# Optimization experiments

Hardware: AMD Instinct MI355X
Metric: run time of the kernel (lower is better)

Reference implementation:

```python
import jax, jax.numpy as jnp
import numpy as np

D_EMBED = 512
NUM_HEADS = 8
HEAD_DIM = D_EMBED // NUM_HEADS
D_FF = 2048
B, L = 2, 4096
LN_EPS = 1e-5


def _layernorm(x, g, b):
    mu = jnp.mean(x, axis=-1, keepdims=True)
    var = jnp.mean(jnp.square(x - mu), axis=-1, keepdims=True)
    return (x - mu) * jax.lax.rsqrt(var + LN_EPS) * g + b


def setup_inputs() -> dict:
    key = jax.random.key(0)
    ks = jax.random.split(key, 16)
    s = 0.02
    inp = {
        "x": jax.random.normal(ks[0], (B, L, D_EMBED), dtype=jnp.float32),
        "mask": jnp.ones((B, 1, 1, L), dtype=jnp.int32),
        # attention projections (stored [in, out] for x @ W)
        "Wq": jax.random.normal(ks[1], (D_EMBED, D_EMBED), dtype=jnp.float32) * s,
        "bq": jnp.zeros((D_EMBED,), dtype=jnp.float32),
        "Wk": jax.random.normal(ks[2], (D_EMBED, D_EMBED), dtype=jnp.float32) * s,
        "bk": jnp.zeros((D_EMBED,), dtype=jnp.float32),
        "Wv": jax.random.normal(ks[3], (D_EMBED, D_EMBED), dtype=jnp.float32) * s,
        "bv": jnp.zeros((D_EMBED,), dtype=jnp.float32),
        "Wo": jax.random.normal(ks[4], (D_EMBED, D_EMBED), dtype=jnp.float32) * s,
        "bo": jnp.zeros((D_EMBED,), dtype=jnp.float32),
        # layernorms
        "ln1_g": jnp.ones((D_EMBED,), dtype=jnp.float32),
        "ln1_b": jnp.zeros((D_EMBED,), dtype=jnp.float32),
        "ln2_g": jnp.ones((D_EMBED,), dtype=jnp.float32),
        "ln2_b": jnp.zeros((D_EMBED,), dtype=jnp.float32),
        # FFN
        "W1": jax.random.normal(ks[5], (D_EMBED, D_FF), dtype=jnp.float32) * s,
        "b1": jnp.zeros((D_FF,), dtype=jnp.float32),
        "W2": jax.random.normal(ks[6], (D_FF, D_EMBED), dtype=jnp.float32) * s,
        "b2": jnp.zeros((D_EMBED,), dtype=jnp.float32),
    }
    return inp


def reference(x, mask, Wq, bq, Wk, bk, Wv, bv, Wo, bo, ln1_g, ln1_b,
              W1, b1, W2, b2, ln2_g, ln2_b):
    Bx, Lx, _ = x.shape
    # projections -> [B, H, L, Dh]
    def split_heads(t):
        return t.reshape(Bx, Lx, NUM_HEADS, HEAD_DIM).transpose(0, 2, 1, 3)
    q = split_heads(x @ Wq + bq)
    k = split_heads(x @ Wk + bk)
    v = split_heads(x @ Wv + bv)
    scores = jnp.einsum("bhqd,bhkd->bhqk", q, k) / jnp.sqrt(
        jnp.asarray(HEAD_DIM, dtype=x.dtype))
    scores = jnp.where(mask == 0, jnp.asarray(-1e9, dtype=x.dtype), scores)
    attn = jax.nn.softmax(scores, axis=-1)
    ctx = jnp.einsum("bhqk,bhkd->bhqd", attn, v)
    ctx = ctx.transpose(0, 2, 1, 3).reshape(Bx, Lx, D_EMBED)
    attn_out = ctx @ Wo + bo

    h = _layernorm(x + attn_out, ln1_g, ln1_b)
    ff = (jax.nn.gelu(h @ W1 + b1, approximate=False)) @ W2 + b2
    return _layernorm(h + ff, ln2_g, ln2_b)
```

## Files before the change

### kernel.cpp

```cpp
#include <hip/hip_runtime.h>
#include <hip/hip_bf16.h>
#include <math.h>

#define D_EMBED 512
#define NUM_HEADS 8
#define HEAD_DIM 64
#define D_FF 2048
#define BATCH 2
#define SEQ 4096
#define M_ROWS (BATCH*SEQ)
#define QSCALE 0.18033688011112042f

typedef __attribute__((ext_vector_type(8))) short short8;
typedef __attribute__((ext_vector_type(4))) short short4_t;
typedef __attribute__((ext_vector_type(4))) float f32x4;

#if __has_builtin(__builtin_amdgcn_mfma_f32_16x16x16bf16_1k)
#define MFMA_K16(a,b,c) __builtin_amdgcn_mfma_f32_16x16x16bf16_1k(a,b,c,0,0,0)
#elif __has_builtin(__builtin_amdgcn_mfma_f32_16x16x16_bf16)
#define MFMA_K16(a,b,c) __builtin_amdgcn_mfma_f32_16x16x16_bf16(a,b,c,0,0,0)
#else
#define MFMA_K16(a,b,c) (c)
#endif

#if __has_builtin(__builtin_amdgcn_exp2f)
#define EXP2(x) __builtin_amdgcn_exp2f(x)
#else
#define EXP2(x) exp2f(x)
#endif

__device__ inline unsigned short f2b(float f) {
    union { float f; unsigned u; } v; v.f = f;
    unsigned r = v.u + 0x7fffu + ((v.u >> 16) & 1u);
    return (unsigned short)(r >> 16);
}

__device__ inline float b2f(short s) {
    union { unsigned u; float f; } v;
    v.u = ((unsigned)(unsigned short)s) << 16;
    return v.f;
}

__device__ inline short4_t pk4(float p0, float p1, float p2, float p3) {
    union { __hip_bfloat162 h2[2]; short4_t s4; } u;
    u.h2[0] = __float22bfloat162_rn(make_float2(p0, p1));
    u.h2[1] = __float22bfloat162_rn(make_float2(p2, p3));
    return u.s4;
}

__device__ inline void gl2lds16(const void* g, void* l) {
    __builtin_amdgcn_global_load_lds(
        (const __attribute__((address_space(1))) unsigned int*)g,
        (__attribute__((address_space(3))) unsigned int*)l, 16, 0, 0);
}

template<int EPI>
__global__ __launch_bounds__(256) void gemm_bt(
    const unsigned short* __restrict__ A, const unsigned short* __restrict__ BT,
    const float* __restrict__ bias, void* __restrict__ Cout,
    int M, int N, int K, int scale_cols)
{
    __shared__ __align__(16) unsigned short As[128*32];
    __shared__ __align__(16) unsigned short Bs[128*32];
    const int tid  = threadIdx.x;
    const int wave = tid >> 6, lane = tid & 63;
    const int wy = wave >> 1, wx = wave & 1;
    const int quad = lane >> 4, m16 = lane & 15;
    const int row0 = blockIdx.y * 128, n0 = blockIdx.x * 128;
    const int rdoff = (quad ^ ((m16 >> 1) & 3)) * 8;

    f32x4 acc[4][4];
#pragma unroll
    for (int i = 0; i < 4; i++)
#pragma unroll
        for (int j = 0; j < 4; j++) acc[i][j] = (f32x4){0.f,0.f,0.f,0.f};

    const int kIters = K >> 5;
    for (int kt = 0; kt < kIters; ++kt) {
        const int k0 = kt << 5;
#pragma unroll
        for (int it = 0; it < 2; ++it) {
            int g  = it*256 + tid;
            int r  = g >> 2;
            int c8 = (((g & 3) ^ ((g >> 3) & 3)) << 3);
            gl2lds16(A  + (size_t)(row0 + r)*K + k0 + c8, &As[(size_t)(it*256 + wave*64)*8]);
            gl2lds16(BT + (size_t)(n0  + r)*K + k0 + c8, &Bs[(size_t)(it*256 + wave*64)*8]);
        }
        __syncthreads();
        short8 a[4], b[4];
#pragma unroll
        for (int i = 0; i < 4; i++) a[i] = *(const short8*)&As[(wy*64 + i*16 + m16)*32 + rdoff];
#pragma unroll
        for (int j = 0; j < 4; j++) b[j] = *(const short8*)&Bs[(wx*64 + j*16 + m16)*32 + rdoff];
#pragma unroll
        for (int i = 0; i < 4; i++)
#pragma unroll
            for (int j = 0; j < 4; j++)
                acc[i][j] = __builtin_amdgcn_mfma_f32_16x16x32_bf16(a[i], b[j], acc[i][j], 0, 0, 0);
        __syncthreads();
    }

#pragma unroll
    for (int j = 0; j < 4; j++) {
        int col = n0 + wx*64 + j*16 + m16;
        float bj = bias[col];
        float sc = (col < scale_cols) ? QSCALE : 1.0f;
#pragma unroll
        for (int i = 0; i < 4; i++) {
            int rbase = row0 + wy*64 + i*16 + quad*4;
#pragma unroll
            for (int r = 0; r < 4; r++) {
                float v = (acc[i][j][r] + bj) * sc;
                size_t idx = (size_t)(rbase + r)*N + col;
                if (EPI == 0) {
                    ((unsigned short*)Cout)[idx] = f2b(v);
                } else if (EPI == 1) {
                    ((float*)Cout)[idx] = v;
                } else {
                    float gv = 0.5f * v * (1.0f + erff(v * 0.70710678118654752f));
                    ((unsigned short*)Cout)[idx] = f2b(gv);
                }
            }
        }
    }
}

template<int EPI>
__global__ __launch_bounds__(256) void gemm_bt64(
    const unsigned short* __restrict__ A, const unsigned short* __restrict__ BT,
    const float* __restrict__ bias, void* __restrict__ Cout,
    int M, int N, int K, int scale_cols)
{
    __shared__ __align__(16) unsigned short As[64*32];
    __shared__ __align__(16) unsigned short Bs[128*32];
    const int tid  = threadIdx.x;
    const int wave = tid >> 6, lane = tid & 63;
    const int wy = wave >> 1, wx = wave & 1;
    const int quad = lane >> 4, m16 = lane & 15;
    const int row0 = blockIdx.y * 64, n0 = blockIdx.x * 128;
    const int rdoff = (quad ^ ((m16 >> 1) & 3)) * 8;

    f32x4 acc[2][4];
#pragma unroll
    for (int i = 0; i < 2; i++)
#pragma unroll
        for (int j = 0; j < 4; j++) acc[i][j] = (f32x4){0.f,0.f,0.f,0.f};

    const int kIters = K >> 5;
    for (int kt = 0; kt < kIters; ++kt) {
        const int k0 = kt << 5;
        {
            int r = tid >> 2;
            int c8 = (((tid & 3) ^ ((tid >> 3) & 3)) << 3);
            gl2lds16(A + (size_t)(row0 + r)*K + k0 + c8, &As[(size_t)(wave*64)*8]);
        }
#pragma unroll
        for (int it = 0; it < 2; ++it) {
            int g  = it*256 + tid;
            int r  = g >> 2;
            int c8 = (((g & 3) ^ ((g >> 3) & 3)) << 3);
            gl2lds16(BT + (size_t)(n0 + r)*K + k0 + c8, &Bs[(size_t)(it*256 + wave*64)*8]);
        }
        __syncthreads();
        short8 a[2], b[4];
#pragma unroll
        for (int i = 0; i < 2; i++) a[i] = *(const short8*)&As[(wy*32 + i*16 + m16)*32 + rdoff];
#pragma unroll
        for (int j = 0; j < 4; j++) b[j] = *(const short8*)&Bs[(wx*64 + j*16 + m16)*32 + rdoff];
#pragma unroll
        for (int i = 0; i < 2; i++)
#pragma unroll
            for (int j = 0; j < 4; j++)
                acc[i][j] = __builtin_amdgcn_mfma_f32_16x16x32_bf16(a[i], b[j], acc[i][j], 0, 0, 0);
        __syncthreads();
    }

#pragma unroll
    for (int j = 0; j < 4; j++) {
        int col = n0 + wx*64 + j*16 + m16;
        float bj = bias[col];
        float sc = (col < scale_cols) ? QSCALE : 1.0f;
#pragma unroll
        for (int i = 0; i < 2; i++) {
            int rbase = row0 + wy*32 + i*16 + quad*4;
#pragma unroll
            for (int r = 0; r < 4; r++) {
                float v = (acc[i][j][r] + bj) * sc;
                size_t idx = (size_t)(rbase + r)*N + col;
                if (EPI == 0) {
                    ((unsigned short*)Cout)[idx] = f2b(v);
                } else if (EPI == 1) {
                    ((float*)Cout)[idx] = v;
                } else {
                    float gv = 0.5f * v * (1.0f + erff(v * 0.70710678118654752f));
                    ((unsigned short*)Cout)[idx] = f2b(gv);
                }
            }
        }
    }
}

__global__ __launch_bounds__(256) void repack_qk(
    const unsigned short* __restrict__ QKV,
    unsigned short* __restrict__ Qp, unsigned short* __restrict__ Kp)
{
    const int bh = blockIdx.y, b = bh >> 3, h = bh & 7;
    const int l0 = blockIdx.x * 64;
    const int t = threadIdx.x;
    const int row = t >> 2, c = (t & 3) * 16;
    const unsigned short* src = QKV + (size_t)(b*SEQ + l0 + row)*1536 + h*64 + c;
    const size_t dst = ((size_t)bh*SEQ + l0 + row)*64 + c;
    *(short8*)&Qp[dst]   = *(const short8*)(src);
    *(short8*)&Qp[dst+8] = *(const short8*)(src + 8);
    *(short8*)&Kp[dst]   = *(const short8*)(src + 512);
    *(short8*)&Kp[dst+8] = *(const short8*)(src + 520);
}

__global__ __launch_bounds__(256) void transpose_v2(
    const unsigned short* __restrict__ QKV, unsigned short* __restrict__ Vp)
{
    __shared__ unsigned short Ls[128][66];
    const int kt = blockIdx.x, bh = blockIdx.y, b = bh >> 3, h = bh & 7;
    const int t = threadIdx.x;
    {
        int key = t >> 1, dhalf = (t & 1) * 32;
        const unsigned short* src =
            QKV + (size_t)(b*SEQ + kt*128 + key)*1536 + 1024 + h*64 + dhalf;
#pragma unroll
        for (int c = 0; c < 4; ++c)
            *(short8*)&Ls[key][dhalf + c*8] = *(const short8*)(src + c*8);
    }
    __syncthreads();
    {
        int quad = t >> 6, d = t & 63;
        unsigned short tmp[32];
#pragma unroll
        for (int nj = 0; nj < 8; ++nj)
#pragma unroll
            for (int r = 0; r < 4; ++r)
                tmp[nj*4 + r] = Ls[nj*16 + quad*4 + r][d];
        unsigned short* dst = Vp + ((((size_t)bh*32 + kt)*4 + quad)*64 + d)*32;
#pragma unroll
        for (int c = 0; c < 4; ++c)
            *(short8*)&dst[c*8] = *(const short8*)&tmp[c*8];
    }
}

__global__ void mask_flags_k(const int* __restrict__ mask, int* __restrict__ flags)
{
    int t = threadIdx.x;
    const int* m = mask + t*128;
    int all = 1;
    for (int i = 0; i < 128; i += 4) {
        int4 v = *(const int4*)(m + i);
        all &= (v.x && v.y && v.z && v.w) ? 1 : 0;
    }
    flags[t] = all;
}

__global__ __launch_bounds__(256) void kmax_k(
    const unsigned short* __restrict__ Kp, float* __restrict__ kmax)
{
    const int bh = blockIdx.x, t = threadIdx.x;
    const int wave = t >> 6, lane = t & 63;
    float mx = 0.f;
    for (int row = t; row < SEQ; row += 256) {
        const unsigned short* kp = Kp + ((size_t)bh*SEQ + row)*64;
        float s = 0.f;
#pragma unroll
        for (int c = 0; c < 8; ++c) {
            short8 v = *(const short8*)(kp + c*8);
#pragma unroll
            for (int j = 0; j < 8; ++j) { float f = b2f(v[j]); s += f*f; }
        }
        mx = fmaxf(mx, s);
    }
#pragma unroll
    for (int off = 32; off >= 1; off >>= 1)
        mx = fmaxf(mx, __shfl_xor(mx, off, 64));
    __shared__ float w[4];
    if (lane == 0) w[wave] = mx;
    __syncthreads();
    if (t == 0)
        kmax[bh] = sqrtf(fmaxf(fmaxf(w[0], w[1]), fmaxf(w[2], w[3])));
}

__global__ __launch_bounds__(256) void flash_attn(
    const unsigned short* __restrict__ Qp, const unsigned short* __restrict__ Kp,
    const unsigned short* __restrict__ Vp, const int* __restrict__ mask,
    const int* __restrict__ flags, const float* __restrict__ kmax,
    unsigned short* __restrict__ O)
{
    __shared__ __align__(16) unsigned short Ks[2][128*32];
    __shared__ __align__(16) unsigned short Vs[4][64*32];
    const int tid = threadIdx.x, wave = tid >> 6, lane = tid & 63;
    const int quad = lane >> 4, m16 = lane & 15;
    const int bh = blockIdx.y, b = bh >> 3, h = bh & 7;
    const int qbase = blockIdx.x * 64 + wave * 16;
    const int fsw = (m16 >> 1) & 3;
    const int koff = (quad ^ fsw) * 8;

    const unsigned short* Qb = Qp + (size_t)bh*SEQ*64;
    const unsigned short* Kb = Kp + (size_t)bh*SEQ*64;
    const unsigned short* Vb = Vp + (size_t)bh*32*4*64*32;
    const int* mbase = mask + b*SEQ;
    const int* fbase = flags + b*(SEQ/128);

    short8 qf[2];
    {
        const unsigned short* qp = Qb + (size_t)(qbase + m16)*64 + quad*8;
        qf[0] = *(const short8*)qp;
        qf[1] = *(const short8*)(qp + 32);
    }
    float qn2 = 0.f;
#pragma unroll
    for (int j = 0; j < 8; ++j) {
        float f0 = b2f(qf[0][j]), f1 = b2f(qf[1][j]);
        qn2 += f0*f0 + f1*f1;
    }
    qn2 += __shfl_xor(qn2, 16, 64);
    qn2 += __shfl_xor(qn2, 32, 64);
    const float M = sqrtf(qn2) * kmax[bh];

    f32x4 accO[4];
#pragma unroll
    for (int dj = 0; dj < 4; dj++) accO[dj] = (f32x4){0.f,0.f,0.f,0.f};
    float rs = 0.f;

    for (int kt = 0; kt < SEQ/128; ++kt) {
        const int key0 = kt * 128;
        const int allones = fbase[kt];
        __syncthreads();
#pragma unroll
        for (int it = 0; it < 2; ++it) {
            int g = it*256 + tid;
            int r = g >> 2;
            int c8 = (((g & 3) ^ ((g >> 3) & 3)) << 3);
            gl2lds16(Kb + (size_t)(key0 + r)*64 + c8,      &Ks[0][(it*256 + wave*64)*8]);
            gl2lds16(Kb + (size_t)(key0 + r)*64 + 32 + c8, &Ks[1][(it*256 + wave*64)*8]);
        }
        {
            int d = wave*16 + (lane >> 2), ch = lane & 3;
            int c8 = (ch ^ ((d >> 1) & 3)) * 8;
#pragma unroll
            for (int qr = 0; qr < 4; ++qr)
                gl2lds16(Vb + (((size_t)kt*4 + qr)*64 + d)*32 + c8,
                         &Vs[qr][wave*64*8]);
        }
        __syncthreads();

        short4_t pb[8];
#pragma unroll
        for (int nj = 0; nj < 8; ++nj) {
            short8 k0 = *(const short8*)&Ks[0][(nj*16 + m16)*32 + koff];
            short8 k1 = *(const short8*)&Ks[1][(nj*16 + m16)*32 + koff];
            f32x4 c = (f32x4){0.f,0.f,0.f,0.f};
            c = __builtin_amdgcn_mfma_f32_16x16x32_bf16(k0, qf[0], c, 0, 0, 0);
            c = __builtin_amdgcn_mfma_f32_16x16x32_bf16(k1, qf[1], c, 0, 0, 0);
            if (!allones) {
                int4 mv = *(const int4*)(mbase + key0 + nj*16 + quad*4);
                c[0] = mv.x ? c[0] : -1e9f;
                c[1] = mv.y ? c[1] : -1e9f;
                c[2] = mv.z ? c[2] : -1e9f;
                c[3] = mv.w ? c[3] : -1e9f;
            }
            float p0 = EXP2(c[0] - M);
            float p1 = EXP2(c[1] - M);
            float p2 = EXP2(c[2] - M);
            float p3 = EXP2(c[3] - M);
            rs += (p0 + p1) + (p2 + p3);
            pb[nj] = pk4(p0, p1, p2, p3);
        }

#pragma unroll
        for (int l = 0; l < 4; ++l) {
#pragma unroll
            for (int dj = 0; dj < 4; ++dj) {
                short8 vv = *(const short8*)
                    &Vs[quad][(dj*16 + m16)*32 + ((l ^ fsw) * 8)];
                short4_t vlo = __builtin_shufflevector(vv, vv, 0, 1, 2, 3);
                short4_t vhi = __builtin_shufflevector(vv, vv, 4, 5, 6, 7);
                accO[dj] = MFMA_K16(vlo, pb[2*l],     accO[dj]);
                accO[dj] = MFMA_K16(vhi, pb[2*l + 1], accO[dj]);
            }
        }
    }

    rs += __shfl_xor(rs, 16, 64);
    rs += __shfl_xor(rs, 32, 64);
    float rl = 1.0f / rs;
#pragma unroll
    for (int dj = 0; dj < 4; ++dj) {
        short4_t o = pk4(accO[dj][0]*rl, accO[dj][1]*rl,
                         accO[dj][2]*rl, accO[dj][3]*rl);
        *(short4_t*)&O[(size_t)(b*SEQ + qbase + m16)*D_EMBED
                       + h*HEAD_DIM + dj*16 + quad*4] = o;
    }
}

__global__ __launch_bounds__(256) void ln_res(
    const float* __restrict__ A, const unsigned short* __restrict__ Bv,
    const float* __restrict__ g, const float* __restrict__ be,
    float* __restrict__ Yf, unsigned short* __restrict__ Yb)
{
    const int wave = threadIdx.x >> 6, lane = threadIdx.x & 63;
    const int row = blockIdx.x * 4 + wave;
    const float* ap = A + (size_t)row*512 + lane*8;
    short8 bv = *(const short8*)(Bv + (size_t)row*512 + lane*8);
    float v[8]; float s = 0.f;
#pragma unroll
    for (int j = 0; j < 8; j++) { v[j] = ap[j] + b2f(bv[j]); s += v[j]; }
#pragma unroll
    for (int off = 32; off >= 1; off >>= 1) s += __shfl_xor(s, off, 64);
    float mu = s * (1.f/512.f);
    float q = 0.f;
#pragma unroll
    for (int j = 0; j < 8; j++) { v[j] -= mu; q += v[j]*v[j]; }
#pragma unroll
    for (int off = 32; off >= 1; off >>= 1) q += __shfl_xor(q, off, 64);
    float rstd = rsqrtf(q * (1.f/512.f) + 1e-5f);
#pragma unroll
    for (int j = 0; j < 8; j++) {
        float y = v[j]*rstd*g[lane*8+j] + be[lane*8+j];
        if (Yf) Yf[(size_t)row*512 + lane*8 + j] = y;
        if (Yb) Yb[(size_t)row*512 + lane*8 + j] = f2b(y);
    }
}

__global__ __launch_bounds__(256) void cvt_f32_bf16(
    const float* __restrict__ X, unsigned short* __restrict__ Y, int n)
{
    int idx = (blockIdx.x * 256 + threadIdx.x) * 4;
    if (idx < n) {
        float4 v = *(const float4*)(X + idx);
        Y[idx+0] = f2b(v.x); Y[idx+1] = f2b(v.y);
        Y[idx+2] = f2b(v.z); Y[idx+3] = f2b(v.w);
    }
}

__global__ void transpose_w(const float* __restrict__ W, unsigned short* __restrict__ WT,
                            int K, int N)
{
    __shared__ float t[32][33];
    int n0 = blockIdx.x*32, k0 = blockIdx.y*32;
    int x = threadIdx.x, y = threadIdx.y;
#pragma unroll
    for (int yy = y; yy < 32; yy += 8) t[yy][x] = W[(size_t)(k0+yy)*N + n0 + x];
    __syncthreads();
#pragma unroll
    for (int yy = y; yy < 32; yy += 8) WT[(size_t)(n0+yy)*K + k0 + x] = f2b(t[x][yy]);
}

__global__ void concat3(const float* __restrict__ a, const float* __restrict__ b,
                        const float* __restrict__ c, float* __restrict__ o)
{
    int i = blockIdx.x*256 + threadIdx.x;
    o[i] = (i < 512) ? a[i] : ((i < 1024) ? b[i-512] : c[i-1024]);
}

extern "C" void kernel_launch(void* const* d_in, const int* in_sizes, int n_in,
                              void* d_out, int out_size, void* d_ws, size_t ws_size,
                              hipStream_t stream)
{
    const float* x    = (const float*)d_in[0];
    const int*   mask = (const int*)  d_in[1];
    const float* Wq = (const float*)d_in[2];  const float* bq = (const float*)d_in[3];
    const float* Wk = (const float*)d_in[4];  const float* bk = (const float*)d_in[5];
    const float* Wv = (const float*)d_in[6];  const float* bv = (const float*)d_in[7];
    const float* Wo = (const float*)d_in[8];  const float* bo = (const float*)d_in[9];
    const float* ln1g = (const float*)d_in[10]; const float* ln1b = (const float*)d_in[11];
    const float* ln2g = (const float*)d_in[12]; const float* ln2b = (const float*)d_in[13];
    const float* W1 = (const float*)d_in[14]; const float* b1 = (const float*)d_in[15];
    const float* W2 = (const float*)d_in[16]; const float* b2 = (const float*)d_in[17];
    float* out = (float*)d_out;

    char* ws = (char*)d_ws;
    const size_t MB = 1024*1024;
    unsigned short* xb    = (unsigned short*)(ws + 0);
    unsigned short* WqkvT = (unsigned short*)(ws + 8*MB);
    unsigned short* W1T   = (unsigned short*)(ws + 10*MB);
    unsigned short* W2T   = (unsigned short*)(ws + 12*MB);
    unsigned short* WoT   = (unsigned short*)(ws + 14*MB);
    float*          bqkv  = (float*)(ws + 14*MB + 512*1024);
    int*            mflag = (int*)(ws + 14*MB + 768*1024);
    float*          kmaxb = (float*)(ws + 14*MB + 772*1024);
    unsigned short* QKVb  = (unsigned short*)(ws + 15*MB);
    unsigned short* Qp    = (unsigned short*)(ws + 39*MB);
    unsigned short* Kp    = (unsigned short*)(ws + 47*MB);
    unsigned short* Vp    = (unsigned short*)(ws + 55*MB);
    unsigned short* ctx   = (unsigned short*)(ws + 63*MB);
    unsigned short* atfb  = (unsigned short*)(ws + 15*MB);
    unsigned short* ffb   = (unsigned short*)(ws + 23*MB);
    float*          hf    = (float*)(ws + 31*MB);
    unsigned short* hb    = (unsigned short*)(ws + 0);
    unsigned short* Gb    = (unsigned short*)(ws + 47*MB);

    dim3 tb(32, 8);
    cvt_f32_bf16<<<4096, 256, 0, stream>>>(x, xb, M_ROWS*D_EMBED);
    transpose_w<<<dim3(16,16), tb, 0, stream>>>(Wq, WqkvT,            512, 512);
    transpose_w<<<dim3(16,16), tb, 0, stream>>>(Wk, WqkvT + 512*512,  512, 512);
    transpose_w<<<dim3(16,16), tb, 0, stream>>>(Wv, WqkvT + 1024*512, 512, 512);
    transpose_w<<<dim3(16,16), tb, 0, stream>>>(Wo, WoT, 512, 512);
    transpose_w<<<dim3(64,16), tb, 0, stream>>>(W1, W1T, 512, 2048);
    transpose_w<<<dim3(16,64), tb, 0, stream>>>(W2, W2T, 2048, 512);
    concat3<<<6, 256, 0, stream>>>(bq, bk, bv, bqkv);
    mask_flags_k<<<1, 64, 0, stream>>>(mask, mflag);

    gemm_bt<0><<<dim3(12,64), 256, 0, stream>>>(xb, WqkvT, bqkv, QKVb, M_ROWS, 1536, 512, 512);

    repack_qk<<<dim3(SEQ/64, 16), 256, 0, stream>>>(QKVb, Qp, Kp);
    transpose_v2<<<dim3(32, 16), 256, 0, stream>>>(QKVb, Vp);
    kmax_k<<<16, 256, 0, stream>>>(Kp, kmaxb);
    flash_attn<<<dim3(SEQ/64, 16), 256, 0, stream>>>(Qp, Kp, Vp, mask, mflag, kmaxb, ctx);

    gemm_bt64<0><<<dim3(4,128), 256, 0, stream>>>(ctx, WoT, bo, atfb, M_ROWS, 512, 512, 0);
    ln_res<<<M_ROWS/4, 256, 0, stream>>>(x, atfb, ln1g, ln1b, hf, hb);

    gemm_bt<2><<<dim3(16,64), 256, 0, stream>>>(hb, W1T, b1, Gb, M_ROWS, D_FF, 512, 0);
    gemm_bt64<0><<<dim3(4,128), 256, 0, stream>>>(Gb, W2T, b2, ffb, M_ROWS, 512, D_FF, 0);
    ln_res<<<M_ROWS/4, 256, 0, stream>>>(hf, ffb, ln2g, ln2b, out, (unsigned short*)nullptr);
}
```

Measured before the change: 431.4 us.

## Fuse QKV head repack and V transpose into QKV GEMM epilogue

```diff
diff --git a/kernel.cpp b/kernel.cpp
--- a/kernel.cpp
+++ b/kernel.cpp
@@ -58,7 +58,7 @@
 __global__ __launch_bounds__(256) void gemm_bt(
     const unsigned short* __restrict__ A, const unsigned short* __restrict__ BT,
     const float* __restrict__ bias, void* __restrict__ Cout,
-    int M, int N, int K, int scale_cols)
+    int M, int N, int K)
 {
     __shared__ __align__(16) unsigned short As[128*32];
     __shared__ __align__(16) unsigned short Bs[128*32];
@@ -104,18 +104,15 @@
     for (int j = 0; j < 4; j++) {
         int col = n0 + wx*64 + j*16 + m16;
         float bj = bias[col];
-        float sc = (col < scale_cols) ? QSCALE : 1.0f;
 #pragma unroll
         for (int i = 0; i < 4; i++) {
             int rbase = row0 + wy*64 + i*16 + quad*4;
 #pragma unroll
             for (int r = 0; r < 4; r++) {
-                float v = (acc[i][j][r] + bj) * sc;
+                float v = acc[i][j][r] + bj;
                 size_t idx = (size_t)(rbase + r)*N + col;
                 if (EPI == 0) {
                     ((unsigned short*)Cout)[idx] = f2b(v);
-                } else if (EPI == 1) {
-                    ((float*)Cout)[idx] = v;
                 } else {
                     float gv = 0.5f * v * (1.0f + erff(v * 0.70710678118654752f));
                     ((unsigned short*)Cout)[idx] = f2b(gv);
@@ -125,11 +122,86 @@
     }
 }
 
-template<int EPI>
+__global__ __launch_bounds__(256) void gemm_qkv(
+    const unsigned short* __restrict__ A, const unsigned short* __restrict__ BT,
+    const float* __restrict__ bias,
+    unsigned short* __restrict__ Qp, unsigned short* __restrict__ Kp,
+    unsigned short* __restrict__ Vp)
+{
+    const int K = 512, N = 1536;
+    __shared__ __align__(16) unsigned short As[128*32];
+    __shared__ __align__(16) unsigned short Bs[128*32];
+    const int tid  = threadIdx.x;
+    const int wave = tid >> 6, lane = tid & 63;
+    const int wy = wave >> 1, wx = wave & 1;
+    const int quad = lane >> 4, m16 = lane & 15;
+    const int row0 = blockIdx.y * 128, n0 = blockIdx.x * 128;
+    const int rdoff = (quad ^ ((m16 >> 1) & 3)) * 8;
+    const int region = n0 >> 9;
+
+    f32x4 acc[4][4];
+#pragma unroll
+    for (int i = 0; i < 4; i++)
+#pragma unroll
+        for (int j = 0; j < 4; j++) acc[i][j] = (f32x4){0.f,0.f,0.f,0.f};
+
+    for (int kt = 0; kt < 16; ++kt) {
+        const int k0 = kt << 5;
+#pragma unroll
+        for (int it = 0; it < 2; ++it) {
+            int g  = it*256 + tid;
+            int r  = g >> 2;
+            int c8 = (((g & 3) ^ ((g >> 3) & 3)) << 3);
+            gl2lds16(A  + (size_t)(row0 + r)*K + k0 + c8, &As[(size_t)(it*256 + wave*64)*8]);
+            gl2lds16(BT + (size_t)(n0  + r)*K + k0 + c8, &Bs[(size_t)(it*256 + wave*64)*8]);
+        }
+        __syncthreads();
+        short8 a[4], b[4];
+#pragma unroll
+        for (int i = 0; i < 4; i++) a[i] = *(const short8*)&As[(wy*64 + i*16 + m16)*32 + rdoff];
+#pragma unroll
+        for (int j = 0; j < 4; j++) b[j] = *(const short8*)&Bs[(wx*64 + j*16 + m16)*32 + rdoff];
+#pragma unroll
+        for (int i = 0; i < 4; i++)
+#pragma unroll
+            for (int j = 0; j < 4; j++)
+                acc[i][j] = __builtin_amdgcn_mfma_f32_16x16x32_bf16(a[i], b[j], acc[i][j], 0, 0, 0);
+        __syncthreads();
+    }
+
+    const float sc = (region == 0) ? QSCALE : 1.0f;
+#pragma unroll
+    for (int j = 0; j < 4; j++) {
+        int col = n0 + wx*64 + j*16 + m16;
+        float bj = bias[col];
+        int cc = col & 511, h = cc >> 6, d = cc & 63;
+#pragma unroll
+        for (int i = 0; i < 4; i++) {
+            int rbase = row0 + wy*64 + i*16 + quad*4;
+#pragma unroll
+            for (int r = 0; r < 4; r++) {
+                float v = (acc[i][j][r] + bj) * sc;
+                int row = rbase + r;
+                int b = row >> 12, l = row & 4095;
+                size_t bh = (size_t)(b*8 + h);
+                if (region == 0) {
+                    Qp[(bh*SEQ + l)*64 + d] = f2b(v);
+                } else if (region == 1) {
+                    Kp[(bh*SEQ + l)*64 + d] = f2b(v);
+                } else {
+                    int kt = l >> 7, kk = l & 127;
+                    int qr = (kk >> 2) & 3, fi = (kk >> 4)*4 + (kk & 3);
+                    Vp[((((bh*32 + kt)*4 + qr)*64 + d)*32) + fi] = f2b(v);
+                }
+            }
+        }
+    }
+}
+
 __global__ __launch_bounds__(256) void gemm_bt64(
     const unsigned short* __restrict__ A, const unsigned short* __restrict__ BT,
-    const float* __restrict__ bias, void* __restrict__ Cout,
-    int M, int N, int K, int scale_cols)
+    const float* __restrict__ bias, unsigned short* __restrict__ Cout,
+    int M, int N, int K)
 {
     __shared__ __align__(16) unsigned short As[64*32];
     __shared__ __align__(16) unsigned short Bs[128*32];
@@ -179,70 +251,15 @@
     for (int j = 0; j < 4; j++) {
         int col = n0 + wx*64 + j*16 + m16;
         float bj = bias[col];
-        float sc = (col < scale_cols) ? QSCALE : 1.0f;
 #pragma unroll
         for (int i = 0; i < 2; i++) {
             int rbase = row0 + wy*32 + i*16 + quad*4;
 #pragma unroll
             for (int r = 0; r < 4; r++) {
-                float v = (acc[i][j][r] + bj) * sc;
-                size_t idx = (size_t)(rbase + r)*N + col;
-                if (EPI == 0) {
-                    ((unsigned short*)Cout)[idx] = f2b(v);
-                } else if (EPI == 1) {
-                    ((float*)Cout)[idx] = v;
-                } else {
-                    float gv = 0.5f * v * (1.0f + erff(v * 0.70710678118654752f));
-                    ((unsigned short*)Cout)[idx] = f2b(gv);
-                }
+                float v = acc[i][j][r] + bj;
+                Cout[(size_t)(rbase + r)*N + col] = f2b(v);
             }
         }
-    }
-}
-
-__global__ __launch_bounds__(256) void repack_qk(
-    const unsigned short* __restrict__ QKV,
-    unsigned short* __restrict__ Qp, unsigned short* __restrict__ Kp)
-{
-    const int bh = blockIdx.y, b = bh >> 3, h = bh & 7;
-    const int l0 = blockIdx.x * 64;
-    const int t = threadIdx.x;
-    const int row = t >> 2, c = (t & 3) * 16;
-    const unsigned short* src = QKV + (size_t)(b*SEQ + l0 + row)*1536 + h*64 + c;
-    const size_t dst = ((size_t)bh*SEQ + l0 + row)*64 + c;
-    *(short8*)&Qp[dst]   = *(const short8*)(src);
-    *(short8*)&Qp[dst+8] = *(const short8*)(src + 8);
-    *(short8*)&Kp[dst]   = *(const short8*)(src + 512);
-    *(short8*)&Kp[dst+8] = *(const short8*)(src + 520);
-}
-
-__global__ __launch_bounds__(256) void transpose_v2(
-    const unsigned short* __restrict__ QKV, unsigned short* __restrict__ Vp)
-{
-    __shared__ unsigned short Ls[128][66];
-    const int kt = blockIdx.x, bh = blockIdx.y, b = bh >> 3, h = bh & 7;
-    const int t = threadIdx.x;
-    {
-        int key = t >> 1, dhalf = (t & 1) * 32;
-        const unsigned short* src =
-            QKV + (size_t)(b*SEQ + kt*128 + key)*1536 + 1024 + h*64 + dhalf;
-#pragma unroll
-        for (int c = 0; c < 4; ++c)
-            *(short8*)&Ls[key][dhalf + c*8] = *(const short8*)(src + c*8);
-    }
-    __syncthreads();
-    {
-        int quad = t >> 6, d = t & 63;
-        unsigned short tmp[32];
-#pragma unroll
-        for (int nj = 0; nj < 8; ++nj)
-#pragma unroll
-            for (int r = 0; r < 4; ++r)
-                tmp[nj*4 + r] = Ls[nj*16 + quad*4 + r][d];
-        unsigned short* dst = Vp + ((((size_t)bh*32 + kt)*4 + quad)*64 + d)*32;
-#pragma unroll
-        for (int c = 0; c < 4; ++c)
-            *(short8*)&dst[c*8] = *(const short8*)&tmp[c*8];
     }
 }
 
@@ -259,36 +276,28 @@
 }
 
 __global__ __launch_bounds__(256) void kmax_k(
-    const unsigned short* __restrict__ Kp, float* __restrict__ kmax)
+    const unsigned short* __restrict__ Kp, unsigned* __restrict__ kmax2)
 {
     const int bh = blockIdx.x, t = threadIdx.x;
-    const int wave = t >> 6, lane = t & 63;
-    float mx = 0.f;
-    for (int row = t; row < SEQ; row += 256) {
-        const unsigned short* kp = Kp + ((size_t)bh*SEQ + row)*64;
-        float s = 0.f;
-#pragma unroll
-        for (int c = 0; c < 8; ++c) {
-            short8 v = *(const short8*)(kp + c*8);
-#pragma unroll
-            for (int j = 0; j < 8; ++j) { float f = b2f(v[j]); s += f*f; }
-        }
-        mx = fmaxf(mx, s);
+    const int row = blockIdx.y*256 + t;
+    const unsigned short* kp = Kp + ((size_t)bh*SEQ + row)*64;
+    float s = 0.f;
+#pragma unroll
+    for (int c = 0; c < 8; ++c) {
+        short8 v = *(const short8*)(kp + c*8);
+#pragma unroll
+        for (int j = 0; j < 8; ++j) { float f = b2f(v[j]); s += f*f; }
     }
 #pragma unroll
     for (int off = 32; off >= 1; off >>= 1)
-        mx = fmaxf(mx, __shfl_xor(mx, off, 64));
-    __shared__ float w[4];
-    if (lane == 0) w[wave] = mx;
-    __syncthreads();
-    if (t == 0)
-        kmax[bh] = sqrtf(fmaxf(fmaxf(w[0], w[1]), fmaxf(w[2], w[3])));
+        s = fmaxf(s, __shfl_xor(s, off, 64));
+    if ((t & 63) == 0) atomicMax(&kmax2[bh], __float_as_uint(s));
 }
 
 __global__ __launch_bounds__(256) void flash_attn(
     const unsigned short* __restrict__ Qp, const unsigned short* __restrict__ Kp,
     const unsigned short* __restrict__ Vp, const int* __restrict__ mask,
-    const int* __restrict__ flags, const float* __restrict__ kmax,
+    const int* __restrict__ flags, const unsigned* __restrict__ kmax2,
     unsigned short* __restrict__ O)
 {
     __shared__ __align__(16) unsigned short Ks[2][128*32];
@@ -320,7 +329,7 @@
     }
     qn2 += __shfl_xor(qn2, 16, 64);
     qn2 += __shfl_xor(qn2, 32, 64);
-    const float M = sqrtf(qn2) * kmax[bh];
+    const float M = sqrtf(qn2 * __uint_as_float(kmax2[bh]));
 
     f32x4 accO[4];
 #pragma unroll
@@ -376,10 +385,9 @@
         for (int l = 0; l < 4; ++l) {
 #pragma unroll
             for (int dj = 0; dj < 4; ++dj) {
-                short8 vv = *(const short8*)
-                    &Vs[quad][(dj*16 + m16)*32 + ((l ^ fsw) * 8)];
-                short4_t vlo = __builtin_shufflevector(vv, vv, 0, 1, 2, 3);
-                short4_t vhi = __builtin_shufflevector(vv, vv, 4, 5, 6, 7);
+                const unsigned short* vrow = &Vs[quad][(dj*16 + m16)*32 + ((l ^ fsw) * 8)];
+                short4_t vlo = *(const short4_t*)vrow;
+                short4_t vhi = *(const short4_t*)(vrow + 4);
                 accO[dj] = MFMA_K16(vlo, pb[2*l],     accO[dj]);
                 accO[dj] = MFMA_K16(vhi, pb[2*l + 1], accO[dj]);
             }
@@ -483,17 +491,16 @@
     unsigned short* WoT   = (unsigned short*)(ws + 14*MB);
     float*          bqkv  = (float*)(ws + 14*MB + 512*1024);
     int*            mflag = (int*)(ws + 14*MB + 768*1024);
-    float*          kmaxb = (float*)(ws + 14*MB + 772*1024);
-    unsigned short* QKVb  = (unsigned short*)(ws + 15*MB);
-    unsigned short* Qp    = (unsigned short*)(ws + 39*MB);
-    unsigned short* Kp    = (unsigned short*)(ws + 47*MB);
-    unsigned short* Vp    = (unsigned short*)(ws + 55*MB);
-    unsigned short* ctx   = (unsigned short*)(ws + 63*MB);
-    unsigned short* atfb  = (unsigned short*)(ws + 15*MB);
-    unsigned short* ffb   = (unsigned short*)(ws + 23*MB);
-    float*          hf    = (float*)(ws + 31*MB);
+    unsigned*       kmaxb = (unsigned*)(ws + 14*MB + 772*1024);
+    unsigned short* Qp    = (unsigned short*)(ws + 15*MB);
+    unsigned short* Kp    = (unsigned short*)(ws + 23*MB);
+    unsigned short* Vp    = (unsigned short*)(ws + 31*MB);
+    unsigned short* ctx   = (unsigned short*)(ws + 39*MB);
+    unsigned short* atfb  = (unsigned short*)(ws + 47*MB);
+    float*          hf    = (float*)(ws + 55*MB);
     unsigned short* hb    = (unsigned short*)(ws + 0);
-    unsigned short* Gb    = (unsigned short*)(ws + 47*MB);
+    unsigned short* Gb    = (unsigned short*)(ws + 15*MB);
+    unsigned short* ffb   = (unsigned short*)(ws + 47*MB);
 
     dim3 tb(32, 8);
     cvt_f32_bf16<<<4096, 256, 0, stream>>>(x, xb, M_ROWS*D_EMBED);
@@ -505,18 +512,17 @@
     transpose_w<<<dim3(16,64), tb, 0, stream>>>(W2, W2T, 2048, 512);
     concat3<<<6, 256, 0, stream>>>(bq, bk, bv, bqkv);
     mask_flags_k<<<1, 64, 0, stream>>>(mask, mflag);
-
-    gemm_bt<0><<<dim3(12,64), 256, 0, stream>>>(xb, WqkvT, bqkv, QKVb, M_ROWS, 1536, 512, 512);
-
-    repack_qk<<<dim3(SEQ/64, 16), 256, 0, stream>>>(QKVb, Qp, Kp);
-    transpose_v2<<<dim3(32, 16), 256, 0, stream>>>(QKVb, Vp);
-    kmax_k<<<16, 256, 0, stream>>>(Kp, kmaxb);
+    hipMemsetAsync(kmaxb, 0, 16*sizeof(unsigned), stream);
+
+    gemm_qkv<<<dim3(12,64), 256, 0, stream>>>(xb, WqkvT, bqkv, Qp, Kp, Vp);
+
+    kmax_k<<<dim3(16,16), 256, 0, stream>>>(Kp, kmaxb);
     flash_attn<<<dim3(SEQ/64, 16), 256, 0, stream>>>(Qp, Kp, Vp, mask, mflag, kmaxb, ctx);
 
-    gemm_bt64<0><<<dim3(4,128), 256, 0, stream>>>(ctx, WoT, bo, atfb, M_ROWS, 512, 512, 0);
+    gemm_bt64<<<dim3(4,128), 256, 0, stream>>>(ctx, WoT, bo, atfb, M_ROWS, 512, 512);
     ln_res<<<M_ROWS/4, 256, 0, stream>>>(x, atfb, ln1g, ln1b, hf, hb);
 
-    gemm_bt<2><<<dim3(16,64), 256, 0, stream>>>(hb, W1T, b1, Gb, M_ROWS, D_FF, 512, 0);
-    gemm_bt64<0><<<dim3(4,128), 256, 0, stream>>>(Gb, W2T, b2, ffb, M_ROWS, 512, D_FF, 0);
+    gemm_bt<2><<<dim3(16,64), 256, 0, stream>>>(hb, W1T, b1, Gb, M_ROWS, D_FF, 512);
+    gemm_bt64<<<dim3(4,128), 256, 0, stream>>>(Gb, W2T, b2, ffb, M_ROWS, 512, D_FF);
     ln_res<<<M_ROWS/4, 256, 0, stream>>>(hf, ffb, ln2g, ln2b, out, (unsigned short*)nullptr);
 }
```

New measurement: 427.9 us. Within noise of the previous version (-0.8%).
